# Kernel optimization log

Measured on AMD Instinct MI355X. Metric: run time of the kernel, lower is better.

The kernel has to match this reference:

```python
import jax, jax.numpy as jnp
import numpy as np


def _blur(x1, kernel):
    # x1: [B,H,W,1], kernel: [k,k,1,1]; 'same' padding conv, stride 1
    return jax.lax.conv_general_dilated(
        x1, kernel, window_strides=(1, 1), padding='SAME',
        dimension_numbers=('NHWC', 'HWIO', 'NHWC'))


def setup_inputs() -> dict:
    key = jax.random.key(0)
    kx, kk = jax.random.split(key)
    B, H, W, C = 32, 512, 512, 3
    KSZ = 9
    x = jax.random.normal(kx, (B, H, W, C), dtype=jnp.float32)
    # Gaussian-random kernel ~ N(1, 0.05), normalized to sum to 1 (as in normal_kernel)
    kernel = 1.0 + 0.05 * jax.random.normal(kk, (KSZ, KSZ, 1, 1), dtype=jnp.float32)
    kernel = kernel / jnp.sum(kernel)
    return {'x': x, 'kernel': kernel}


def reference(x, kernel):
    # conv2d helper in the original convolves each channel with the SAME kernel
    # then averages across channels; that equals convolving the channel-mean once.
    local_mean = _blur(jnp.mean(x, axis=-1, keepdims=True), kernel)   # [B,H,W,1]
    v = x - local_mean                                                # [B,H,W,C]
    sigma = jnp.sqrt(_blur(jnp.mean(jnp.square(v), axis=-1, keepdims=True), kernel))  # [B,H,W,1]
    mean_sigma = jnp.mean(sigma, axis=(1, 2), keepdims=True)          # [B,1,1,1]
    return v / jnp.maximum(mean_sigma, sigma)
```

## Files before the change

kernel.cpp:

```cpp
#include <hip/hip_runtime.h>

#define BB 32
#define HH 512
#define WW 512
#define HW (HH * WW)
#define NPIX (BB * HH * WW)

#define TILE 64
#define RG 72
#define RQ 19
#define RS 76
#define NQ (RG * 18)

#define LOADROW12(dst, p4, base)                                              \
    {                                                                         \
        float4 A_ = (p4)[base], B_ = (p4)[(base) + 1], C_ = (p4)[(base) + 2]; \
        (dst)[0] = A_.x; (dst)[1] = A_.y; (dst)[2]  = A_.z; (dst)[3]  = A_.w; \
        (dst)[4] = B_.x; (dst)[5] = B_.y; (dst)[6]  = B_.z; (dst)[7]  = B_.w; \
        (dst)[8] = C_.x; (dst)[9] = C_.y; (dst)[10] = C_.z; (dst)[11] = C_.w; \
    }

#define BLUR_4x4(acc, t4, kw, tx, ty)                                         \
    float fw[4][12];                                                          \
    _Pragma("unroll")                                                         \
    for (int j = 0; j < 3; ++j) LOADROW12(fw[j], t4, (4 * (ty) + j) * RQ + (tx)); \
    _Pragma("unroll")                                                         \
    for (int ky = 0; ky < 9; ++ky) {                                          \
        LOADROW12(fw[(ky + 3) & 3], t4, (4 * (ty) + ky + 3) * RQ + (tx));     \
        float w[9];                                                           \
        _Pragma("unroll")                                                     \
        for (int kx = 0; kx < 9; ++kx) w[kx] = kw[ky * 9 + kx];               \
        _Pragma("unroll")                                                     \
        for (int my = 0; my < 4; ++my)                                        \
            _Pragma("unroll")                                                 \
            for (int kx = 0; kx < 9; ++kx)                                    \
                _Pragma("unroll")                                             \
                for (int mx = 0; mx < 4; ++mx)                                \
                    acc[my][mx] = fmaf(w[kx], fw[(my + ky) & 3][mx + kx], acc[my][mx]); \
    }

__global__ __launch_bounds__(256) void k_lme(const float* __restrict__ x,
                                             const float* __restrict__ kw,
                                             float* __restrict__ lm,
                                             float* __restrict__ eb) {
    __shared__ float mt[RG * RS];
    const int tx = threadIdx.x, ty = threadIdx.y;
    const int tid = ty * 16 + tx;
    const int x0 = blockIdx.x * TILE, y0 = blockIdx.y * TILE;
    const size_t boff = (size_t)blockIdx.z * HW;
    const float4* x4 = (const float4*)(x + boff * 3);

    for (int i = tid; i < NQ; i += 256) {
        int r = i / 18, q = i - r * 18;
        int gy = y0 + r - 4, gx = x0 + 4 * q - 4;
        float4 m = make_float4(0.f, 0.f, 0.f, 0.f);
        if (gy >= 0 && gy < HH && gx >= 0 && gx < WW) {
            int go = (gy * WW + gx) >> 2;
            float4 a = x4[3 * go + 0];
            float4 b = x4[3 * go + 1];
            float4 c = x4[3 * go + 2];
            const float t = 1.f / 3.f;
            m.x = (a.x + a.y + a.z) * t;
            m.y = (a.w + b.x + b.y) * t;
            m.z = (b.z + b.w + c.x) * t;
            m.w = (c.y + c.z + c.w) * t;
        }
        *(float4*)&mt[r * RS + 4 * q] = m;
    }
    __syncthreads();

    const float4* t4 = (const float4*)mt;
    float acc[4][4] = {};
    BLUR_4x4(acc, t4, kw, tx, ty);

    float* lp = lm + boff + (size_t)(y0 + 4 * ty) * WW + x0 + 4 * tx;
    float* ep = eb + boff + (size_t)(y0 + 4 * ty) * WW + x0 + 4 * tx;
#pragma unroll
    for (int my = 0; my < 4; ++my) {
        float4 l = make_float4(acc[my][0], acc[my][1], acc[my][2], acc[my][3]);
        *(float4*)(lp + my * WW) = l;
        int gy = y0 + 4 * ty + my, gx = x0 + 4 * tx;
        int go = (gy * WW + gx) >> 2;
        float4 a = x4[3 * go + 0];
        float4 b = x4[3 * go + 1];
        float4 c = x4[3 * go + 2];
        const float t = 1.f / 3.f;
        float4 m, q, e;
        m.x = (a.x + a.y + a.z) * t;  q.x = (a.x * a.x + a.y * a.y + a.z * a.z) * t;
        m.y = (a.w + b.x + b.y) * t;  q.y = (a.w * a.w + b.x * b.x + b.y * b.y) * t;
        m.z = (b.z + b.w + c.x) * t;  q.z = (b.z * b.z + b.w * b.w + c.x * c.x) * t;
        m.w = (c.y + c.z + c.w) * t;  q.w = (c.y * c.y + c.z * c.z + c.w * c.w) * t;
        e.x = fmaxf(q.x - l.x * (2.f * m.x - l.x), 0.f);
        e.y = fmaxf(q.y - l.y * (2.f * m.y - l.y), 0.f);
        e.z = fmaxf(q.z - l.z * (2.f * m.z - l.z), 0.f);
        e.w = fmaxf(q.w - l.w * (2.f * m.w - l.w), 0.f);
        *(float4*)(ep + my * WW) = e;
    }
}

__global__ __launch_bounds__(256) void k_sigma(const float* __restrict__ eb,
                                               const float* __restrict__ kw,
                                               float* __restrict__ sg,
                                               float* __restrict__ psums) {
    __shared__ float et[RG * RS];
    __shared__ float wsum[4];
    const int tx = threadIdx.x, ty = threadIdx.y;
    const int tid = ty * 16 + tx;
    const int x0 = blockIdx.x * TILE, y0 = blockIdx.y * TILE;
    const size_t boff = (size_t)blockIdx.z * HW;
    const float4* e4 = (const float4*)(eb + boff);

    for (int i = tid; i < NQ; i += 256) {
        int r = i / 18, q = i - r * 18;
        int gy = y0 + r - 4, gx = x0 + 4 * q - 4;
        float4 e = make_float4(0.f, 0.f, 0.f, 0.f);
        if (gy >= 0 && gy < HH && gx >= 0 && gx < WW)
            e = e4[(gy * WW + gx) >> 2];
        *(float4*)&et[r * RS + 4 * q] = e;
    }
    __syncthreads();

    const float4* t4 = (const float4*)et;
    float acc[4][4] = {};
    BLUR_4x4(acc, t4, kw, tx, ty);

    float s = 0.f;
    float* dp = sg + boff + (size_t)(y0 + 4 * ty) * WW + x0 + 4 * tx;
#pragma unroll
    for (int my = 0; my < 4; ++my) {
        float4 o;
        o.x = sqrtf(fmaxf(acc[my][0], 0.f));
        o.y = sqrtf(fmaxf(acc[my][1], 0.f));
        o.z = sqrtf(fmaxf(acc[my][2], 0.f));
        o.w = sqrtf(fmaxf(acc[my][3], 0.f));
        *(float4*)(dp + my * WW) = o;
        s += o.x + o.y + o.z + o.w;
    }
#pragma unroll
    for (int off = 32; off > 0; off >>= 1) s += __shfl_down(s, off);
    if ((tid & 63) == 0) wsum[tid >> 6] = s;
    __syncthreads();
    if (tid == 0)
        psums[blockIdx.z * 64 + blockIdx.y * 8 + blockIdx.x] =
            wsum[0] + wsum[1] + wsum[2] + wsum[3];
}

__global__ __launch_bounds__(256) void k_norm(const float4* __restrict__ x4,
                                              const float4* __restrict__ lm4,
                                              const float4* __restrict__ sg4,
                                              const float* __restrict__ psums,
                                              float4* __restrict__ out4) {
    __shared__ float msh;
    int g = blockIdx.x * 256 + threadIdx.x;
    int b = g >> 16;
    float s = 0.f;
    if (threadIdx.x < 64) s = psums[b * 64 + threadIdx.x];
#pragma unroll
    for (int off = 32; off > 0; off >>= 1) s += __shfl_down(s, off);
    if (threadIdx.x == 0) msh = s * (1.f / (float)HW);
    __syncthreads();
    float ms = msh;

    float4 l = lm4[g];
    float4 sv = sg4[g];
    float i0 = 1.f / fmaxf(ms, sv.x);
    float i1 = 1.f / fmaxf(ms, sv.y);
    float i2 = 1.f / fmaxf(ms, sv.z);
    float i3 = 1.f / fmaxf(ms, sv.w);
    float4 a = x4[3 * g + 0];
    float4 bb = x4[3 * g + 1];
    float4 c = x4[3 * g + 2];
    float4 o0, o1, o2;
    o0.x = (a.x - l.x) * i0;  o0.y = (a.y - l.x) * i0;  o0.z = (a.z - l.x) * i0;
    o0.w = (a.w - l.y) * i1;  o1.x = (bb.x - l.y) * i1; o1.y = (bb.y - l.y) * i1;
    o1.z = (bb.z - l.z) * i2; o1.w = (bb.w - l.z) * i2; o2.x = (c.x - l.z) * i2;
    o2.y = (c.y - l.w) * i3;  o2.z = (c.z - l.w) * i3;  o2.w = (c.w - l.w) * i3;
    out4[3 * g + 0] = o0;
    out4[3 * g + 1] = o1;
    out4[3 * g + 2] = o2;
}

extern "C" void kernel_launch(void* const* d_in, const int* in_sizes, int n_in,
                              void* d_out, int out_size, void* d_ws, size_t ws_size,
                              hipStream_t stream) {
    const float* x = (const float*)d_in[0];
    const float* kw = (const float*)d_in[1];
    float* out = (float*)d_out;
    float* wsp = (float*)d_ws;
    float* lmb = wsp;
    float* sgb = wsp + (size_t)NPIX;
    float* ebb = wsp + 2 * (size_t)NPIX;
    float* ps  = wsp + 3 * (size_t)NPIX;

    dim3 blk(16, 16);
    dim3 grd(WW / TILE, HH / TILE, BB);
    k_lme<<<grd, blk, 0, stream>>>(x, kw, lmb, ebb);
    k_sigma<<<grd, blk, 0, stream>>>(ebb, kw, sgb, ps);

    k_norm<<<NPIX / 4 / 256, 256, 0, stream>>>((const float4*)x, (const float4*)lmb,
                                               (const float4*)sgb, ps, (float4*)out);
}
```

Before: 263.7 us.

## Fuse local-mean and sigma blur kernels with halo recompute in shared memory

Merges the two blur kernels into one. Each 64x64 tile loads an 80x80 channel-mean halo and computes the first blur over a 72x72 region, recomputing the overlap with neighbouring tiles. The resulting squared-deviation field stays in shared memory for the second blur. This removes the global write and reread of the intermediate e buffer and one kernel launch. In exchange it does about 27% more first-blur work, reloads x for the halo region, adds extra barriers, and leaves some threads idle during the second partial pass.

```diff
diff --git a/kernel.cpp b/kernel.cpp
--- a/kernel.cpp
+++ b/kernel.cpp
@@ -7,10 +7,11 @@
 #define NPIX (BB * HH * WW)
 
 #define TILE 64
-#define RG 72
-#define RQ 19
-#define RS 76
-#define NQ (RG * 18)
+#define MQ 21
+#define MS 84
+#define MR 80
+#define EQ 19
+#define ES 76
 
 #define LOADROW12(dst, p4, base)                                              \
     {                                                                         \
@@ -20,109 +21,118 @@
         (dst)[8] = C_.x; (dst)[9] = C_.y; (dst)[10] = C_.z; (dst)[11] = C_.w; \
     }
 
-#define BLUR_4x4(acc, t4, kw, tx, ty)                                         \
-    float fw[4][12];                                                          \
-    _Pragma("unroll")                                                         \
-    for (int j = 0; j < 3; ++j) LOADROW12(fw[j], t4, (4 * (ty) + j) * RQ + (tx)); \
-    _Pragma("unroll")                                                         \
-    for (int ky = 0; ky < 9; ++ky) {                                          \
-        LOADROW12(fw[(ky + 3) & 3], t4, (4 * (ty) + ky + 3) * RQ + (tx));     \
-        float w[9];                                                           \
+#define BLUR9(acc, p4, r0, sq, c0)                                            \
+    {                                                                         \
+        float fw[4][12];                                                      \
         _Pragma("unroll")                                                     \
-        for (int kx = 0; kx < 9; ++kx) w[kx] = kw[ky * 9 + kx];               \
+        for (int j = 0; j < 3; ++j) LOADROW12(fw[j], p4, ((r0) + j) * (sq) + (c0)); \
         _Pragma("unroll")                                                     \
-        for (int my = 0; my < 4; ++my)                                        \
+        for (int ky = 0; ky < 9; ++ky) {                                      \
+            LOADROW12(fw[(ky + 3) & 3], p4, ((r0) + ky + 3) * (sq) + (c0));   \
+            float w[9];                                                       \
             _Pragma("unroll")                                                 \
-            for (int kx = 0; kx < 9; ++kx)                                    \
+            for (int kx = 0; kx < 9; ++kx) w[kx] = kw[ky * 9 + kx];           \
+            _Pragma("unroll")                                                 \
+            for (int my = 0; my < 4; ++my)                                    \
                 _Pragma("unroll")                                             \
-                for (int mx = 0; mx < 4; ++mx)                                \
-                    acc[my][mx] = fmaf(w[kx], fw[(my + ky) & 3][mx + kx], acc[my][mx]); \
-    }
-
-__global__ __launch_bounds__(256) void k_lme(const float* __restrict__ x,
-                                             const float* __restrict__ kw,
-                                             float* __restrict__ lm,
-                                             float* __restrict__ eb) {
-    __shared__ float mt[RG * RS];
+                for (int kx = 0; kx < 9; ++kx)                                \
+                    _Pragma("unroll")                                         \
+                    for (int mx = 0; mx < 4; ++mx)                            \
+                        acc[my][mx] = fmaf(w[kx], fw[(my + ky) & 3][mx + kx], acc[my][mx]); \
+        }                                                                     \
+    }
+
+__global__ __launch_bounds__(256, 5) void k_stats(const float* __restrict__ x,
+                                                  const float* __restrict__ kw,
+                                                  float* __restrict__ lm,
+                                                  float* __restrict__ sg,
+                                                  float* __restrict__ psums) {
+    __shared__ float smem[MR * MS];
+    __shared__ float wsum[4];
     const int tx = threadIdx.x, ty = threadIdx.y;
     const int tid = ty * 16 + tx;
     const int x0 = blockIdx.x * TILE, y0 = blockIdx.y * TILE;
     const size_t boff = (size_t)blockIdx.z * HW;
     const float4* x4 = (const float4*)(x + boff * 3);
-
-    for (int i = tid; i < NQ; i += 256) {
-        int r = i / 18, q = i - r * 18;
-        int gy = y0 + r - 4, gx = x0 + 4 * q - 4;
+    float* lmg = lm + boff;
+
+    for (int i = tid; i < MR * 20; i += 256) {
+        int r = i / 20, q = i - r * 20;
+        int gy = y0 + r - 8, gx = x0 + 4 * q - 8;
         float4 m = make_float4(0.f, 0.f, 0.f, 0.f);
         if (gy >= 0 && gy < HH && gx >= 0 && gx < WW) {
             int go = (gy * WW + gx) >> 2;
-            float4 a = x4[3 * go + 0];
-            float4 b = x4[3 * go + 1];
-            float4 c = x4[3 * go + 2];
+            float4 a = x4[3 * go + 0], b = x4[3 * go + 1], c = x4[3 * go + 2];
             const float t = 1.f / 3.f;
             m.x = (a.x + a.y + a.z) * t;
             m.y = (a.w + b.x + b.y) * t;
             m.z = (b.z + b.w + c.x) * t;
             m.w = (c.y + c.z + c.w) * t;
         }
-        *(float4*)&mt[r * RS + 4 * q] = m;
-    }
-    __syncthreads();
-
-    const float4* t4 = (const float4*)mt;
+        *(float4*)&smem[r * MS + 4 * q] = m;
+    }
+    __syncthreads();
+
+    const float4* m4 = (const float4*)smem;
+
+    auto tileA = [&](int t, float (&eo)[4][4]) {
+        int tr = t / 18, q0 = t - tr * 18;
+        float acc[4][4] = {};
+        BLUR9(acc, m4, 4 * tr, MQ, q0);
+        const int X0 = x0 - 4 + 4 * q0;
+        const bool cin = (X0 >= 0) && (X0 < WW);
+        const bool wlm = (tr >= 1) && (tr <= 16) && (q0 >= 1) && (q0 <= 16);
+#pragma unroll
+        for (int row = 0; row < 4; ++row) {
+            int Y = y0 - 4 + 4 * tr + row;
+            float4 l = make_float4(acc[row][0], acc[row][1], acc[row][2], acc[row][3]);
+            if (wlm) *(float4*)(lmg + (size_t)Y * WW + X0) = l;
+            float4 e = make_float4(0.f, 0.f, 0.f, 0.f);
+            if (cin && Y >= 0 && Y < HH) {
+                float4 mm = *(const float4*)&smem[(4 * tr + row + 4) * MS + 4 * (q0 + 1)];
+                int go = (Y * WW + X0) >> 2;
+                float4 a = x4[3 * go + 0], b = x4[3 * go + 1], c = x4[3 * go + 2];
+                const float t3 = 1.f / 3.f;
+                float4 qv;
+                qv.x = (a.x * a.x + a.y * a.y + a.z * a.z) * t3;
+                qv.y = (a.w * a.w + b.x * b.x + b.y * b.y) * t3;
+                qv.z = (b.z * b.z + b.w * b.w + c.x * c.x) * t3;
+                qv.w = (c.y * c.y + c.z * c.z + c.w * c.w) * t3;
+                e.x = fmaxf(qv.x - l.x * (2.f * mm.x - l.x), 0.f);
+                e.y = fmaxf(qv.y - l.y * (2.f * mm.y - l.y), 0.f);
+                e.z = fmaxf(qv.z - l.z * (2.f * mm.z - l.z), 0.f);
+                e.w = fmaxf(qv.w - l.w * (2.f * mm.w - l.w), 0.f);
+            }
+            eo[row][0] = e.x; eo[row][1] = e.y; eo[row][2] = e.z; eo[row][3] = e.w;
+        }
+    };
+
+    float e1[4][4];
+    tileA(tid, e1);
+    __syncthreads();
+
+    {
+        int tr = tid / 18, q0 = tid - tr * 18;
+#pragma unroll
+        for (int row = 0; row < 4; ++row)
+            *(float4*)&smem[(4 * tr + row) * ES + 4 * q0] =
+                make_float4(e1[row][0], e1[row][1], e1[row][2], e1[row][3]);
+    }
+    float e2[4][4];
+    if (tid < 68) tileA(256 + tid, e2);
+    __syncthreads();
+    if (tid < 68) {
+        int t = 256 + tid, tr = t / 18, q0 = t - tr * 18;
+#pragma unroll
+        for (int row = 0; row < 4; ++row)
+            *(float4*)&smem[(4 * tr + row) * ES + 4 * q0] =
+                make_float4(e2[row][0], e2[row][1], e2[row][2], e2[row][3]);
+    }
+    __syncthreads();
+
+    const float4* e4s = (const float4*)smem;
     float acc[4][4] = {};
-    BLUR_4x4(acc, t4, kw, tx, ty);
-
-    float* lp = lm + boff + (size_t)(y0 + 4 * ty) * WW + x0 + 4 * tx;
-    float* ep = eb + boff + (size_t)(y0 + 4 * ty) * WW + x0 + 4 * tx;
-#pragma unroll
-    for (int my = 0; my < 4; ++my) {
-        float4 l = make_float4(acc[my][0], acc[my][1], acc[my][2], acc[my][3]);
-        *(float4*)(lp + my * WW) = l;
-        int gy = y0 + 4 * ty + my, gx = x0 + 4 * tx;
-        int go = (gy * WW + gx) >> 2;
-        float4 a = x4[3 * go + 0];
-        float4 b = x4[3 * go + 1];
-        float4 c = x4[3 * go + 2];
-        const float t = 1.f / 3.f;
-        float4 m, q, e;
-        m.x = (a.x + a.y + a.z) * t;  q.x = (a.x * a.x + a.y * a.y + a.z * a.z) * t;
-        m.y = (a.w + b.x + b.y) * t;  q.y = (a.w * a.w + b.x * b.x + b.y * b.y) * t;
-        m.z = (b.z + b.w + c.x) * t;  q.z = (b.z * b.z + b.w * b.w + c.x * c.x) * t;
-        m.w = (c.y + c.z + c.w) * t;  q.w = (c.y * c.y + c.z * c.z + c.w * c.w) * t;
-        e.x = fmaxf(q.x - l.x * (2.f * m.x - l.x), 0.f);
-        e.y = fmaxf(q.y - l.y * (2.f * m.y - l.y), 0.f);
-        e.z = fmaxf(q.z - l.z * (2.f * m.z - l.z), 0.f);
-        e.w = fmaxf(q.w - l.w * (2.f * m.w - l.w), 0.f);
-        *(float4*)(ep + my * WW) = e;
-    }
-}
-
-__global__ __launch_bounds__(256) void k_sigma(const float* __restrict__ eb,
-                                               const float* __restrict__ kw,
-                                               float* __restrict__ sg,
-                                               float* __restrict__ psums) {
-    __shared__ float et[RG * RS];
-    __shared__ float wsum[4];
-    const int tx = threadIdx.x, ty = threadIdx.y;
-    const int tid = ty * 16 + tx;
-    const int x0 = blockIdx.x * TILE, y0 = blockIdx.y * TILE;
-    const size_t boff = (size_t)blockIdx.z * HW;
-    const float4* e4 = (const float4*)(eb + boff);
-
-    for (int i = tid; i < NQ; i += 256) {
-        int r = i / 18, q = i - r * 18;
-        int gy = y0 + r - 4, gx = x0 + 4 * q - 4;
-        float4 e = make_float4(0.f, 0.f, 0.f, 0.f);
-        if (gy >= 0 && gy < HH && gx >= 0 && gx < WW)
-            e = e4[(gy * WW + gx) >> 2];
-        *(float4*)&et[r * RS + 4 * q] = e;
-    }
-    __syncthreads();
-
-    const float4* t4 = (const float4*)et;
-    float acc[4][4] = {};
-    BLUR_4x4(acc, t4, kw, tx, ty);
+    BLUR9(acc, e4s, 4 * ty, EQ, tx);
 
     float s = 0.f;
     float* dp = sg + boff + (size_t)(y0 + 4 * ty) * WW + x0 + 4 * tx;
@@ -189,13 +199,11 @@
     float* wsp = (float*)d_ws;
     float* lmb = wsp;
     float* sgb = wsp + (size_t)NPIX;
-    float* ebb = wsp + 2 * (size_t)NPIX;
-    float* ps  = wsp + 3 * (size_t)NPIX;
+    float* ps  = wsp + 2 * (size_t)NPIX;
 
     dim3 blk(16, 16);
     dim3 grd(WW / TILE, HH / TILE, BB);
-    k_lme<<<grd, blk, 0, stream>>>(x, kw, lmb, ebb);
-    k_sigma<<<grd, blk, 0, stream>>>(ebb, kw, sgb, ps);
+    k_stats<<<grd, blk, 0, stream>>>(x, kw, lmb, sgb, ps);
 
     k_norm<<<NPIX / 4 / 256, 256, 0, stream>>>((const float4*)x, (const float4*)lmb,
                                                (const float4*)sgb, ps, (float4*)out);
```

After: 692.7 us. +162.6%, slower.
